# Kernel optimization log

Hardware: AMD Instinct MI355X
Metric: run time of the kernel (lower is better)

Reference implementation:

```python
import jax, jax.numpy as jnp
import numpy as np

B, S, HID = 1, 2048, 2048
H, KVH, D = 32, 8, 64
NUM_MASKS = 3
ROPE_THETA = 10000.0


def rope_tables(seq_len, dim, theta=ROPE_THETA):
    inv_freq = 1.0 / (theta ** (np.arange(0, dim, 2, dtype=np.float32) / dim))
    t = np.arange(seq_len, dtype=np.float32)
    freqs = np.outer(t, inv_freq)                      # [S, D/2]
    emb = np.concatenate([freqs, freqs], axis=-1)      # [S, D]
    return jnp.asarray(np.cos(emb))[None], jnp.asarray(np.sin(emb))[None]  # [1,S,D]


def setup_inputs() -> dict:
    key = jax.random.key(0)
    ks = jax.random.split(key, 5)
    cos, sin = rope_tables(S, D)
    sc = 1.0 / np.sqrt(HID)
    return {
        "hidden_states": jax.random.normal(ks[0], (B, S, HID), jnp.float32),
        "cos": cos, "sin": sin,
        "Wq": jax.random.normal(ks[1], (HID, H * D), jnp.float32) * sc,
        "Wk": jax.random.normal(ks[2], (HID, KVH * D), jnp.float32) * sc,
        "Wv": jax.random.normal(ks[3], (HID, KVH * D), jnp.float32) * sc,
        "Wo": jax.random.normal(ks[4], (H * D, HID), jnp.float32) * sc,
        "num_masks": NUM_MASKS,
    }


def rotate_half(x):
    x1, x2 = jnp.split(x, 2, axis=-1)
    return jnp.concatenate([-x2, x1], axis=-1)


def block_causal_bias(seq_len, num_mask, dtype):
    block_size = num_mask + 1
    i = jnp.arange(seq_len)[:, None]
    j = jnp.arange(seq_len)[None, :]
    causal = j <= i
    column = causal & (j % (num_mask + 1) == 0)
    block = causal & ((i // block_size) == (j // block_size))
    allowed = column | block
    neg = jnp.asarray(jnp.finfo(dtype).min if dtype != jnp.float32 else -jnp.inf, dtype)
    return jnp.where(allowed, jnp.asarray(0.0, dtype), neg)  # [S,S]


def reference(hidden_states, cos, sin, Wq, Wk, Wv, Wo, num_masks):
    b, s, _ = hidden_states.shape
    scaling = D ** -0.5
    # projections -> [B, heads, S, D]
    q = (hidden_states @ Wq).reshape(b, s, H, D).transpose(0, 2, 1, 3)
    k = (hidden_states @ Wk).reshape(b, s, KVH, D).transpose(0, 2, 1, 3)
    v = (hidden_states @ Wv).reshape(b, s, KVH, D).transpose(0, 2, 1, 3)
    # RoPE (cos/sin: [1,S,D] -> [1,1,S,D])
    c, sn = cos[:, None], sin[:, None]
    q = q * c + rotate_half(q) * sn
    k = k * c + rotate_half(k) * sn
    # GQA: repeat kv heads
    g = H // KVH
    k = jnp.repeat(k, g, axis=1)
    v = jnp.repeat(v, g, axis=1)
    bias = block_causal_bias(s, num_masks, hidden_states.dtype)  # [S,S]
    scores = jnp.einsum("bhqd,bhkd->bhqk", q, k) * scaling + bias[None, None]
    probs = jax.nn.softmax(scores, axis=-1)
    out = jnp.einsum("bhqk,bhkd->bhqd", probs, v)  # [B,H,S,D]
    out = out.transpose(0, 2, 1, 3).reshape(b, s, H * D)
    return out @ Wo
```

## Files before the change

### kernel.cpp

```cpp
#include <hip/hip_runtime.h>
#include <hip/hip_bf16.h>
#include <stdint.h>

#define S_LEN  2048
#define HIDDEN 2048
#define NH     32
#define NKVH   8
#define HD     64
#define NHD    (NH*HD)
#define KVD    (NKVH*HD)

typedef __attribute__((ext_vector_type(8))) short  short8;
typedef __attribute__((ext_vector_type(4))) short  short4v;
typedef __attribute__((ext_vector_type(4))) float  f32x4;
typedef __attribute__((ext_vector_type(4))) float  float4v;
typedef __attribute__((ext_vector_type(8))) __bf16 bf16x8;

__device__ __forceinline__ short f2bf(float x){
  uint32_t u = __builtin_bit_cast(uint32_t, x);
  u += 0x7fffu + ((u >> 16) & 1u);
  return (short)(u >> 16);
}

__device__ __forceinline__ f32x4 mfma_bf16(short8 a, short8 b, f32x4 c){
  return __builtin_amdgcn_mfma_f32_16x16x32_bf16(
      __builtin_bit_cast(bf16x8, a), __builtin_bit_cast(bf16x8, b), c, 0, 0, 0);
}

__device__ __forceinline__ void gload16(const short* g, short* l){
  __builtin_amdgcn_global_load_lds(
      (const __attribute__((address_space(1))) void*)g,
      (__attribute__((address_space(3))) void*)l, 16, 0, 0);
}

__global__ __launch_bounds__(256) void k_prep(const float* __restrict__ hs,
                                              short* __restrict__ hsb,
                                              const float* __restrict__ Wq, short* __restrict__ WqT,
                                              const float* __restrict__ Wk, short* __restrict__ WkT,
                                              const float* __restrict__ Wv, short* __restrict__ WvT,
                                              const float* __restrict__ Wo, short* __restrict__ WoT){
  int bid = blockIdx.x;
  if (bid < 4096){
    int i = bid*256 + threadIdx.x;
    float4v v = ((const float4v* __restrict__)hs)[i];
    short4v o;
#pragma unroll
    for (int j=0;j<4;j++) o[j] = f2bf(v[j]);
    ((short4v* __restrict__)hsb)[i] = o;
    return;
  }
  bid -= 4096;
  const float* W; short* WT; int R, C, GX;
  if (bid < 4096)      { W = Wq; WT = WqT; R = HIDDEN; C = NHD; GX = 64; }
  else if (bid < 5120) { bid -= 4096; W = Wk; WT = WkT; R = HIDDEN; C = KVD; GX = 16; }
  else if (bid < 6144) { bid -= 5120; W = Wv; WT = WvT; R = HIDDEN; C = KVD; GX = 16; }
  else                 { bid -= 6144; W = Wo; WT = WoT; R = NHD; C = HIDDEN; GX = 64; }
  const int bx = bid % GX, by = bid / GX;
  __shared__ float tile[32][33];
  const int x = threadIdx.x & 31, y0 = threadIdx.x >> 5;
  const int c0 = bx*32, r0 = by*32;
#pragma unroll
  for (int yy=y0; yy<32; yy+=8) tile[yy][x] = W[(size_t)(r0+yy)*C + c0 + x];
  __syncthreads();
#pragma unroll
  for (int yy=y0; yy<32; yy+=8) WT[(size_t)(c0+yy)*R + r0 + x] = f2bf(tile[x][yy]);
}

struct GemmIdx {
  int wid, r, g, wr, wc, kg, gtid;
};
__device__ __forceinline__ GemmIdx gemm_idx(){
  GemmIdx ix;
  int tid = threadIdx.x, lane = tid&63;
  ix.kg = tid>>8; ix.gtid = tid&255;
  ix.wid = (tid>>6)&3; ix.r = lane&15; ix.g = lane>>4;
  ix.wr = ix.wid>>1; ix.wc = ix.wid&1;
  return ix;
}

__device__ __forceinline__ void stage128(const short* gA, const short* gB,
                                         short* As, short* Bs, int kt, int w){
  const int K = HIDDEN;
  gload16(gA + kt*32,                As + w*512);
  gload16(gA + (size_t)64*K + kt*32, As + 2048 + w*512);
  gload16(gB + kt*32,                Bs + w*512);
  gload16(gB + (size_t)64*K + kt*32, Bs + 2048 + w*512);
}

__device__ __forceinline__ void compute128(const short* As, const short* Bs,
                                           f32x4 acc[4][4], const GemmIdx& ix){
  short8 af[4], bf[4];
#pragma unroll
  for (int m=0;m<4;m++) af[m] = *(const short8*)&As[(ix.wr*64 + m*16 + ix.r)*32 + ix.g*8];
#pragma unroll
  for (int n=0;n<4;n++) bf[n] = *(const short8*)&Bs[(ix.wc*64 + n*16 + ix.r)*32 + ix.g*8];
#pragma unroll
  for (int m=0;m<4;m++)
#pragma unroll
    for (int n=0;n<4;n++) acc[m][n] = mfma_bf16(af[m], bf[n], acc[m][n]);
}

template<int NG, int NKT>
__device__ __forceinline__ void gemm_core512(const short* __restrict__ A,
                                             const short* __restrict__ BT,
                                             int bm, int bn, short* LDS,
                                             f32x4 acc[4][4], const GemmIdx& ix){
  const int K = HIDDEN;
  const short* gA = A  + (size_t)(bm*128 + (ix.gtid>>2))*K + ix.kg*(NKT*32) + (ix.gtid&3)*8;
  const short* gB = BT + (size_t)(bn*128 + (ix.gtid>>2))*K + ix.kg*(NKT*32) + (ix.gtid&3)*8;
  short* L   = LDS + ix.kg*16384;
  short* As0 = L;        short* Bs0 = L + 4096;
  short* As1 = L + 8192; short* Bs1 = L + 12288;
  const int w = ix.gtid>>6;

#pragma unroll
  for (int m=0;m<4;m++)
#pragma unroll
    for (int n=0;n<4;n++) acc[m][n] = (f32x4){0.f,0.f,0.f,0.f};

  stage128(gA, gB, As0, Bs0, 0, w);
  __syncthreads();
  for (int u=0; u<NKT/2; ++u){
    const int t = 2*u;
    if (t+1 < NKT) stage128(gA, gB, As1, Bs1, t+1, w);
    compute128(As0, Bs0, acc, ix);
    __syncthreads();
    if (t+2 < NKT) stage128(gA, gB, As0, Bs0, t+2, w);
    compute128(As1, Bs1, acc, ix);
    __syncthreads();
  }

  float* red = (float*)LDS;
#pragma unroll
  for (int src=1; src<NG; ++src){
    __syncthreads();
    if (ix.kg == src){
#pragma unroll
      for (int m=0;m<4;m++)
#pragma unroll
        for (int n=0;n<4;n++)
#pragma unroll
          for (int j=0;j<4;j++)
            red[ix.wid*4096 + (m*16 + ix.g*4 + j)*64 + n*16 + ix.r] = acc[m][n][j];
    }
    __syncthreads();
    if (ix.kg == 0){
#pragma unroll
      for (int m=0;m<4;m++)
#pragma unroll
        for (int n=0;n<4;n++)
#pragma unroll
          for (int j=0;j<4;j++)
            acc[m][n][j] += red[ix.wid*4096 + (m*16 + ix.g*4 + j)*64 + n*16 + ix.r];
    }
  }
}

__global__ __launch_bounds__(512, 4) void k_gemm_qkv(const short* __restrict__ hsb,
                                                     const short* __restrict__ WqT,
                                                     const short* __restrict__ WkT,
                                                     const short* __restrict__ WvT,
                                                     const float* __restrict__ cosT,
                                                     const float* __restrict__ sinT,
                                                     const int* __restrict__ nm,
                                                     short* __restrict__ Qb,
                                                     short* __restrict__ Kb,
                                                     short* __restrict__ VT,
                                                     short* __restrict__ VTs){
  __shared__ short LDS[32768];
  const int bn = blockIdx.x, bm = blockIdx.y;
  GemmIdx ix = gemm_idx();
  f32x4 acc[4][4];

  if (bn < 16){
    gemm_core512<2,32>(hsb, WqT + (size_t)bn*128*HIDDEN, bm, 0, LDS, acc, ix);
    if (ix.kg) return;
    const int h2 = bn*2 + ix.wc;
#pragma unroll
    for (int m=0;m<4;m++)
#pragma unroll
      for (int j=0;j<4;j++){
        const int s = bm*128 + ix.wr*64 + m*16 + ix.g*4 + j;
        const float* cr = cosT + s*64;
        const float* sr = sinT + s*64;
#pragma unroll
        for (int n=0;n<2;n++){
          const int d = n*16 + ix.r;
          float x1 = acc[m][n][j], x2 = acc[m][n+2][j];
          Qb[(size_t)s*NHD + h2*64 + d]      = f2bf((x1*cr[d]    - x2*sr[d])   *0.125f);
          Qb[(size_t)s*NHD + h2*64 + d + 32] = f2bf((x2*cr[d+32] + x1*sr[d+32])*0.125f);
        }
      }
  } else if (bn < 20){
    gemm_core512<2,32>(hsb, WkT + (size_t)(bn-16)*128*HIDDEN, bm, 0, LDS, acc, ix);
    if (ix.kg) return;
    const int h2 = (bn-16)*2 + ix.wc;
#pragma unroll
    for (int m=0;m<4;m++)
#pragma unroll
      for (int j=0;j<4;j++){
        const int s = bm*128 + ix.wr*64 + m*16 + ix.g*4 + j;
        const float* cr = cosT + s*64;
        const float* sr = sinT + s*64;
#pragma unroll
        for (int n=0;n<2;n++){
          const int d = n*16 + ix.r;
          float x1 = acc[m][n][j], x2 = acc[m][n+2][j];
          Kb[(size_t)s*KVD + h2*64 + d]      = f2bf(x1*cr[d]    - x2*sr[d]);
          Kb[(size_t)s*KVD + h2*64 + d + 32] = f2bf(x2*cr[d+32] + x1*sr[d+32]);
        }
      }
  } else {
    gemm_core512<2,32>(hsb, WvT + (size_t)(bn-20)*128*HIDDEN, bm, 0, LDS, acc, ix);
    const int bs  = nm[0] + 1;
    const int lbs = 31 - __clz(bs);
    const int d0  = (bn-20)*128;
    const int s0  = bm*128;
    short* Vt = LDS;
    __syncthreads();
    if (!ix.kg){
#pragma unroll
      for (int n=0;n<4;n++){
        const int dr = ix.wc*64 + n*16 + ix.r;
#pragma unroll
        for (int m=0;m<4;m++){
          const int sc_ = ix.wr*64 + m*16 + ix.g*4;
          short4v o;
#pragma unroll
          for (int j=0;j<4;j++) o[j] = f2bf(acc[m][n][j]);
          *(short4v*)&Vt[dr*136 + sc_] = o;
        }
      }
    }
    __syncthreads();
    const int tid = threadIdx.x;
#pragma unroll
    for (int it=0; it<4; ++it){
      const int row = tid>>2, c8 = (tid&3)*32 + it*8;
      *(short8*)&VT[(size_t)(d0+row)*S_LEN + s0 + c8] = *(short8*)&Vt[row*136 + c8];
    }
    const int cnt = 128 >> lbs;
    for (int e = tid; e < 128*cnt; e += 512){
      const int row = e >> (7 - lbs), c = e & (cnt - 1);
      VTs[(size_t)(d0+row)*S_LEN + (s0>>lbs) + c] = Vt[row*136 + (c<<lbs)];
    }
  }
}

__global__ __launch_bounds__(1024, 4) void k_gemm(const short* __restrict__ A,
                                                  const short* __restrict__ BT,
                                                  float* __restrict__ C, int Nc){
  __shared__ short LDS[65536];
  const int bn = blockIdx.x, bm = blockIdx.y;
  GemmIdx ix = gemm_idx();
  f32x4 acc[4][4];
  gemm_core512<4,16>(A, BT, bm, bn, LDS, acc, ix);
  if (ix.kg) return;
#pragma unroll
  for (int m=0;m<4;m++)
#pragma unroll
    for (int n=0;n<4;n++)
#pragma unroll
      for (int j=0;j<4;j++)
        C[(size_t)(bm*128 + ix.wr*64 + m*16 + ix.g*4 + j)*Nc
          + bn*128 + ix.wc*64 + n*16 + ix.r] = acc[m][n][j];
}


__device__ __forceinline__ void sm_pv1(f32x4 sc[4],
                                       float mrow[4], float lrow[4],
                                       f32x4 acc[4], short* Pw,
                                       const short* Vtile,
                                       int r, int g){
#pragma unroll
  for (int j=0;j<4;j++){
    float v = fmaxf(fmaxf(sc[0][j], sc[1][j]), fmaxf(sc[2][j], sc[3][j]));
    v = fmaxf(v, __shfl_xor(v, 1));
    v = fmaxf(v, __shfl_xor(v, 2));
    v = fmaxf(v, __shfl_xor(v, 4));
    v = fmaxf(v, __shfl_xor(v, 8));
    float mn = fmaxf(mrow[j], v);
    float fac = __expf(mrow[j] - mn);
    mrow[j] = mn;
#pragma unroll
    for (int f=0;f<4;f++) acc[f][j] *= fac;
    float rs = 0.f;
#pragma unroll
    for (int n=0;n<4;n++){
      float p = __expf(sc[n][j] - mn);
      rs += p;
      sc[n][j] = p;
    }
    rs += __shfl_xor(rs, 1);
    rs += __shfl_xor(rs, 2);
    rs += __shfl_xor(rs, 4);
    rs += __shfl_xor(rs, 8);
    lrow[j] = lrow[j]*fac + rs;
  }
#pragma unroll
  for (int n=0;n<4;n++)
#pragma unroll
    for (int j=0;j<4;j++)
      Pw[(g*4+j)*72 + n*16 + r] = f2bf(sc[n][j]);

  short8 pf0 = *(short8*)&Pw[r*72 + g*8];
  short8 pf1 = *(short8*)&Pw[r*72 + 32 + g*8];
#pragma unroll
  for (int f=0;f<4;f++){
    short8 vf0 = *(const short8*)(Vtile + (size_t)(f*16 + r)*S_LEN + g*8);
    short8 vf1 = *(const short8*)(Vtile + (size_t)(f*16 + r)*S_LEN + 32 + g*8);
    acc[f] = mfma_bf16(pf0, vf0, acc[f]);
    acc[f] = mfma_bf16(pf1, vf1, acc[f]);
  }
}

__global__ __launch_bounds__(64, 4) void k_attn3(const short* __restrict__ Qb,
                                                 const short* __restrict__ Kb,
                                                 const short* __restrict__ VT,
                                                 const short* __restrict__ VTs,
                                                 const int* __restrict__ nm,
                                                 short* __restrict__ Ob){
  const int i  = gridDim.x - 1 - blockIdx.x;
  const int qs = i >> 5;
  const int h  = i & 31;
  const int hk = h >> 2;
  const int bs = nm[0] + 1;

  const int lane = threadIdx.x;
  const int r = lane&15, g = lane>>4;

  __shared__ short Pw[16*72];

  const int qlo = qs*16;

  short8 qf0 = *(const short8*)(Qb + (size_t)(qlo + r)*NHD + h*HD + g*8);
  short8 qf1 = *(const short8*)(Qb + (size_t)(qlo + r)*NHD + h*HD + 32 + g*8);

  f32x4 acc[4];
  float mrow[4], lrow[4];
#pragma unroll
  for (int f=0;f<4;f++) acc[f] = (f32x4){0.f,0.f,0.f,0.f};
#pragma unroll
  for (int j=0;j<4;j++){ mrow[j] = -1e30f; lrow[j] = 0.f; }

  const short* Kg  = Kb  + hk*HD;
  const short* Vsg = VTs + (size_t)hk*HD*S_LEN;
  const short* Vdg = VT  + (size_t)hk*HD*S_LEN;

  const int cmax = qlo / bs;
  const int nct = (cmax + 63) >> 6;
  for (int ct=0; ct<nct; ++ct){
    const int cbase = ct*64;
    f32x4 sc[4];
#pragma unroll
    for (int n=0;n<4;n++){
      const int key = bs*(cbase + n*16 + r);
      short8 kf0 = *(const short8*)(Kg + (size_t)key*KVD + g*8);
      short8 kf1 = *(const short8*)(Kg + (size_t)key*KVD + 32 + g*8);
      f32x4 z = (f32x4){0.f,0.f,0.f,0.f};
      z = mfma_bf16(qf0, kf0, z);
      sc[n] = mfma_bf16(qf1, kf1, z);
    }
    if (cmax - cbase < 64){
#pragma unroll
      for (int n=0;n<4;n++){
        if (cbase + n*16 + r >= cmax){
#pragma unroll
          for (int j=0;j<4;j++) sc[n][j] = -1e30f;
        }
      }
    }
    sm_pv1(sc, mrow, lrow, acc, Pw, Vsg + cbase, r, g);
  }

  {
    const int key = qlo + r;
    short8 kf0 = *(const short8*)(Kg + (size_t)key*KVD + g*8);
    short8 kf1 = *(const short8*)(Kg + (size_t)key*KVD + 32 + g*8);
    f32x4 z = (f32x4){0.f,0.f,0.f,0.f};
    z = mfma_bf16(qf0, kf0, z);
    f32x4 sc0 = mfma_bf16(qf1, kf1, z);

    const int rb = r / bs, rm = r % bs;
#pragma unroll
    for (int j=0;j<4;j++){
      const int qrel = g*4 + j;
      bool ok = (r <= qrel) && ((rm == 0) || (rb == qrel/bs));
      sc0[j] = ok ? sc0[j] : -1e30f;
    }

#pragma unroll
    for (int j=0;j<4;j++){
      float v = sc0[j];
      v = fmaxf(v, __shfl_xor(v, 1));
      v = fmaxf(v, __shfl_xor(v, 2));
      v = fmaxf(v, __shfl_xor(v, 4));
      v = fmaxf(v, __shfl_xor(v, 8));
      float mn = fmaxf(mrow[j], v);
      float fac = __expf(mrow[j] - mn);
      mrow[j] = mn;
#pragma unroll
      for (int f=0;f<4;f++) acc[f][j] *= fac;
      float p = __expf(sc0[j] - mn);
      sc0[j] = p;
      float rs = p;
      rs += __shfl_xor(rs, 1);
      rs += __shfl_xor(rs, 2);
      rs += __shfl_xor(rs, 4);
      rs += __shfl_xor(rs, 8);
      lrow[j] = lrow[j]*fac + rs;
    }
#pragma unroll
    for (int j=0;j<4;j++){
      Pw[(g*4+j)*72 + r]      = f2bf(sc0[j]);
      Pw[(g*4+j)*72 + 16 + r] = 0;
    }
    short8 pf0 = *(short8*)&Pw[r*72 + g*8];
#pragma unroll
    for (int f=0;f<4;f++){
      short8 vf0 = *(const short8*)(Vdg + (size_t)(f*16 + r)*S_LEN + qlo + g*8);
      acc[f] = mfma_bf16(pf0, vf0, acc[f]);
    }
  }

#pragma unroll
  for (int j=0;j<4;j++){
    float inv = 1.f / lrow[j];
    const int q = qlo + g*4 + j;
#pragma unroll
    for (int f=0;f<4;f++)
      Ob[(size_t)q*NHD + h*HD + f*16 + r] = f2bf(acc[f][j]*inv);
  }
}

extern "C" void kernel_launch(void* const* d_in, const int* in_sizes, int n_in,
                              void* d_out, int out_size, void* d_ws, size_t ws_size,
                              hipStream_t stream){
  const float* hs   = (const float*)d_in[0];
  const float* cosT = (const float*)d_in[1];
  const float* sinT = (const float*)d_in[2];
  const float* Wq   = (const float*)d_in[3];
  const float* Wk   = (const float*)d_in[4];
  const float* Wv   = (const float*)d_in[5];
  const float* Wo   = (const float*)d_in[6];
  const int*   nm   = (const int*)d_in[7];

  char* ws = (char*)d_ws;
  short* hsb  = (short*)(ws);
  short* WqT  = (short*)(ws + (8ull<<20));
  short* WkT  = (short*)(ws + (16ull<<20));
  short* WvT  = (short*)(ws + (18ull<<20));
  short* WoT  = (short*)(ws + (20ull<<20));
  short* Qb   = (short*)(ws + (28ull<<20));
  short* Kb   = (short*)(ws + (36ull<<20));
  short* VT   = (short*)(ws + (38ull<<20));
  short* VTs  = (short*)(ws + (40ull<<20));
  short* attnb= (short*)(ws + (42ull<<20));
  float* out  = (float*)d_out;

  k_prep<<<dim3(14336), 256, 0, stream>>>(hs, hsb, Wq, WqT, Wk, WkT, Wv, WvT, Wo, WoT);

  k_gemm_qkv<<<dim3(24, 16), 512, 0, stream>>>(hsb, WqT, WkT, WvT, cosT, sinT, nm,
                                               Qb, Kb, VT, VTs);

  k_attn3<<<dim3((S_LEN/16)*NH), 64, 0, stream>>>(Qb, Kb, VT, VTs, nm, attnb);

  k_gemm<<<dim3(NHD/128, S_LEN/128), 1024, 0, stream>>>(attnb, WoT, out, HIDDEN);
}
```

Measured before the change: 130.8 us.

## Triple-buffer GEMM K-loop with vmcnt waits and use 2-way split-K for output GEMM

Replaces the double-buffered GEMM main loop with a three-stage LDS ring. Each iteration issues its async global-to-LDS loads two tiles ahead, then waits with explicit s_waitcnt vmcnt and raw s_barrier instead of __syncthreads. This is meant to hide global load latency behind the MFMA work. The output projection GEMM drops from 4-way split-K with 1024 threads to 2-way with 512 threads, which shortens the reduction but leaves fewer waves per block and uses more LDS per group.

```diff
diff --git a/kernel.cpp b/kernel.cpp
--- a/kernel.cpp
+++ b/kernel.cpp
@@ -15,6 +15,11 @@
 typedef __attribute__((ext_vector_type(4))) float  f32x4;
 typedef __attribute__((ext_vector_type(4))) float  float4v;
 typedef __attribute__((ext_vector_type(8))) __bf16 bf16x8;
+
+#define WAITVM8()  asm volatile("s_waitcnt vmcnt(8)" ::: "memory")
+#define WAITVM4()  asm volatile("s_waitcnt vmcnt(4)" ::: "memory")
+#define WAITVM0()  asm volatile("s_waitcnt vmcnt(0)" ::: "memory")
+#define ABARRIER() asm volatile("s_barrier" ::: "memory")
 
 __device__ __forceinline__ short f2bf(float x){
   uint32_t u = __builtin_bit_cast(uint32_t, x);
@@ -78,15 +83,6 @@
   return ix;
 }
 
-__device__ __forceinline__ void stage128(const short* gA, const short* gB,
-                                         short* As, short* Bs, int kt, int w){
-  const int K = HIDDEN;
-  gload16(gA + kt*32,                As + w*512);
-  gload16(gA + (size_t)64*K + kt*32, As + 2048 + w*512);
-  gload16(gB + kt*32,                Bs + w*512);
-  gload16(gB + (size_t)64*K + kt*32, Bs + 2048 + w*512);
-}
-
 __device__ __forceinline__ void compute128(const short* As, const short* Bs,
                                            f32x4 acc[4][4], const GemmIdx& ix){
   short8 af[4], bf[4];
@@ -100,17 +96,15 @@
     for (int n=0;n<4;n++) acc[m][n] = mfma_bf16(af[m], bf[n], acc[m][n]);
 }
 
-template<int NG, int NKT>
-__device__ __forceinline__ void gemm_core512(const short* __restrict__ A,
-                                             const short* __restrict__ BT,
-                                             int bm, int bn, short* LDS,
-                                             f32x4 acc[4][4], const GemmIdx& ix){
+template<int NKT>
+__device__ __forceinline__ void gemm_core(const short* __restrict__ A,
+                                          const short* __restrict__ BT,
+                                          int bm, int bn, short* LDS,
+                                          f32x4 acc[4][4], const GemmIdx& ix){
   const int K = HIDDEN;
   const short* gA = A  + (size_t)(bm*128 + (ix.gtid>>2))*K + ix.kg*(NKT*32) + (ix.gtid&3)*8;
   const short* gB = BT + (size_t)(bn*128 + (ix.gtid>>2))*K + ix.kg*(NKT*32) + (ix.gtid&3)*8;
-  short* L   = LDS + ix.kg*16384;
-  short* As0 = L;        short* Bs0 = L + 4096;
-  short* As1 = L + 8192; short* Bs1 = L + 12288;
+  short* L = LDS + ix.kg*24576;
   const int w = ix.gtid>>6;
 
 #pragma unroll
@@ -118,41 +112,55 @@
 #pragma unroll
     for (int n=0;n<4;n++) acc[m][n] = (f32x4){0.f,0.f,0.f,0.f};
 
-  stage128(gA, gB, As0, Bs0, 0, w);
+  auto STAGE = [&](int buf, int kt){
+    short* As_ = L + buf*8192;
+    gload16(gA + kt*32,                As_ + w*512);
+    gload16(gA + (size_t)64*K + kt*32, As_ + 2048 + w*512);
+    gload16(gB + kt*32,                As_ + 4096 + w*512);
+    gload16(gB + (size_t)64*K + kt*32, As_ + 6144 + w*512);
+  };
+
+  STAGE(0, 0);
+  STAGE(1, 1);
+  int cur = 0;
+  for (int t=0; t<NKT-2; ++t){
+    int nxt = cur+2; if (nxt>=3) nxt-=3;
+    STAGE(nxt, t+2);
+    WAITVM8();
+    ABARRIER();
+    compute128(L + cur*8192, L + cur*8192 + 4096, acc, ix);
+    ABARRIER();
+    cur = (cur==2) ? 0 : cur+1;
+  }
+  WAITVM4();
+  ABARRIER();
+  compute128(L + cur*8192, L + cur*8192 + 4096, acc, ix);
+  ABARRIER();
+  cur = (cur==2) ? 0 : cur+1;
+  WAITVM0();
+  ABARRIER();
+  compute128(L + cur*8192, L + cur*8192 + 4096, acc, ix);
+
   __syncthreads();
-  for (int u=0; u<NKT/2; ++u){
-    const int t = 2*u;
-    if (t+1 < NKT) stage128(gA, gB, As1, Bs1, t+1, w);
-    compute128(As0, Bs0, acc, ix);
-    __syncthreads();
-    if (t+2 < NKT) stage128(gA, gB, As0, Bs0, t+2, w);
-    compute128(As1, Bs1, acc, ix);
-    __syncthreads();
-  }
-
   float* red = (float*)LDS;
-#pragma unroll
-  for (int src=1; src<NG; ++src){
-    __syncthreads();
-    if (ix.kg == src){
-#pragma unroll
-      for (int m=0;m<4;m++)
-#pragma unroll
-        for (int n=0;n<4;n++)
-#pragma unroll
-          for (int j=0;j<4;j++)
-            red[ix.wid*4096 + (m*16 + ix.g*4 + j)*64 + n*16 + ix.r] = acc[m][n][j];
-    }
-    __syncthreads();
-    if (ix.kg == 0){
-#pragma unroll
-      for (int m=0;m<4;m++)
-#pragma unroll
-        for (int n=0;n<4;n++)
-#pragma unroll
-          for (int j=0;j<4;j++)
-            acc[m][n][j] += red[ix.wid*4096 + (m*16 + ix.g*4 + j)*64 + n*16 + ix.r];
-    }
+  if (ix.kg){
+#pragma unroll
+    for (int m=0;m<4;m++)
+#pragma unroll
+      for (int n=0;n<4;n++)
+#pragma unroll
+        for (int j=0;j<4;j++)
+          red[ix.wid*4096 + (m*16 + ix.g*4 + j)*64 + n*16 + ix.r] = acc[m][n][j];
+  }
+  __syncthreads();
+  if (!ix.kg){
+#pragma unroll
+    for (int m=0;m<4;m++)
+#pragma unroll
+      for (int n=0;n<4;n++)
+#pragma unroll
+        for (int j=0;j<4;j++)
+          acc[m][n][j] += red[ix.wid*4096 + (m*16 + ix.g*4 + j)*64 + n*16 + ix.r];
   }
 }
 
@@ -167,13 +175,13 @@
                                                      short* __restrict__ Kb,
                                                      short* __restrict__ VT,
                                                      short* __restrict__ VTs){
-  __shared__ short LDS[32768];
+  __shared__ short LDS[49152];
   const int bn = blockIdx.x, bm = blockIdx.y;
   GemmIdx ix = gemm_idx();
   f32x4 acc[4][4];
 
   if (bn < 16){
-    gemm_core512<2,32>(hsb, WqT + (size_t)bn*128*HIDDEN, bm, 0, LDS, acc, ix);
+    gemm_core<32>(hsb, WqT + (size_t)bn*128*HIDDEN, bm, 0, LDS, acc, ix);
     if (ix.kg) return;
     const int h2 = bn*2 + ix.wc;
 #pragma unroll
@@ -192,7 +200,7 @@
         }
       }
   } else if (bn < 20){
-    gemm_core512<2,32>(hsb, WkT + (size_t)(bn-16)*128*HIDDEN, bm, 0, LDS, acc, ix);
+    gemm_core<32>(hsb, WkT + (size_t)(bn-16)*128*HIDDEN, bm, 0, LDS, acc, ix);
     if (ix.kg) return;
     const int h2 = (bn-16)*2 + ix.wc;
 #pragma unroll
@@ -211,7 +219,7 @@
         }
       }
   } else {
-    gemm_core512<2,32>(hsb, WvT + (size_t)(bn-20)*128*HIDDEN, bm, 0, LDS, acc, ix);
+    gemm_core<32>(hsb, WvT + (size_t)(bn-20)*128*HIDDEN, bm, 0, LDS, acc, ix);
     const int bs  = nm[0] + 1;
     const int lbs = 31 - __clz(bs);
     const int d0  = (bn-20)*128;
@@ -247,14 +255,14 @@
   }
 }
 
-__global__ __launch_bounds__(1024, 4) void k_gemm(const short* __restrict__ A,
-                                                  const short* __restrict__ BT,
-                                                  float* __restrict__ C, int Nc){
-  __shared__ short LDS[65536];
+__global__ __launch_bounds__(512, 4) void k_gemm(const short* __restrict__ A,
+                                                 const short* __restrict__ BT,
+                                                 float* __restrict__ C, int Nc){
+  __shared__ short LDS[49152];
   const int bn = blockIdx.x, bm = blockIdx.y;
   GemmIdx ix = gemm_idx();
   f32x4 acc[4][4];
-  gemm_core512<4,16>(A, BT, bm, bn, LDS, acc, ix);
+  gemm_core<32>(A, BT, bm, bn, LDS, acc, ix);
   if (ix.kg) return;
 #pragma unroll
   for (int m=0;m<4;m++)
@@ -465,5 +473,5 @@
 
   k_attn3<<<dim3((S_LEN/16)*NH), 64, 0, stream>>>(Qb, Kb, VT, VTs, nm, attnb);
 
-  k_gemm<<<dim3(NHD/128, S_LEN/128), 1024, 0, stream>>>(attnb, WoT, out, HIDDEN);
-}
+  k_gemm<<<dim3(NHD/128, S_LEN/128), 512, 0, stream>>>(attnb, WoT, out, HIDDEN);
+}
```

New measurement: 135.6 us. 3.6% more time.
